# Optimization experiments

Hardware: AMD Instinct MI355X
Metric: run time of the kernel (lower is better)

## Reference

```python
import jax, jax.numpy as jnp
import numpy as np

N, E, B = 4096, 32768, 64
F_IN, E_FEAT, D, D3, G = 128, 64, 64, 64, 10
L = 3           # gc_count
SIG = 0.15      # prior_sig
LAMDA = 0.01    # DiffGroupNorm lambda
EPS = 1e-5      # BatchNorm eps


def setup_inputs() -> dict:
    key = jax.random.key(0)
    ks = jax.random.split(key, 24)
    u = lambda k, shape, s=0.02: jax.random.uniform(k, shape, jnp.float32, -s, s)
    return {
        "x": jax.random.normal(ks[0], (N, F_IN), jnp.float32),
        "edge_attr": jax.random.normal(ks[1], (E, E_FEAT), jnp.float32),
        "pre_W": u(ks[2], (F_IN, D)),
        "pre_b": u(ks[3], (D,)),
        "edge_w1": u(ks[4], (L, E_FEAT, D3), 0.1),
        "edge_b1": u(ks[5], (L, D3), 0.1),
        "edge_w2": u(ks[6], (L, D3, D * D), 0.05),
        "edge_b2": u(ks[7], (L, D * D), 0.05),
        "root_w": u(ks[8], (L, D, D), 0.1),
        "root_b": u(ks[9], (L, D), 0.1),
        "gru_wih": u(ks[10], (L, 3 * D, D), 0.1),
        "gru_whh": u(ks[11], (L, 3 * D, D), 0.1),
        "gru_bih": u(ks[12], (L, 3 * D), 0.1),
        "gru_bhh": u(ks[13], (L, 3 * D), 0.1),
        "gn_lin": u(ks[14], (L, D, G), 0.1),
        "gn_gamma": jnp.ones((L, G * D), jnp.float32),
        "gn_beta": jnp.zeros((L, G * D), jnp.float32),
        "post_W": u(ks[15], (D, D)),
        "post_b": u(ks[16], (D,)),
        "out_W": u(ks[17], (D, 1)),
        "out_b": u(ks[18], (1,)),
        "edge_index": jax.random.randint(ks[19], (2, E), 0, N),
        "batch": jnp.sort(jax.random.randint(ks[20], (N,), 0, B)),
    }


def _kld_det(W, b):
    # BayesLinear forward with sample=False: closed-form prior term
    logc = jnp.log(SIG * jnp.sqrt(2.0 * np.pi))
    return (0.5 * (W / SIG) ** 2 + logc).sum() + (0.5 * (b / SIG) ** 2 + logc).sum()


def _seg_mean(v, idx, num):
    s = jax.ops.segment_sum(v, idx, num_segments=num)
    c = jax.ops.segment_sum(jnp.ones((v.shape[0],), v.dtype), idx, num_segments=num)
    return s / jnp.clip(c, 1.0)[:, None]


def _gru_cell(m, h, wih, whh, bih, bhh):
    # torch GRU gate order: r, z, n
    gi = m @ wih.T + bih          # [N, 3D]
    gh = h @ whh.T + bhh
    i_r, i_z, i_n = jnp.split(gi, 3, axis=-1)
    h_r, h_z, h_n = jnp.split(gh, 3, axis=-1)
    r = jax.nn.sigmoid(i_r + h_r)
    z = jax.nn.sigmoid(i_z + h_z)
    n = jnp.tanh(i_n + r * h_n)
    return (1.0 - z) * n + z * h


def _diff_group_norm(m, lin, gamma, beta):
    # PyG DiffGroupNorm: x + lamda * sum_g s[:,g] * BN(s*x)
    s = jax.nn.softmax(m @ lin, axis=-1)           # [N, G]
    t = (s[:, :, None] * m[:, None, :]).reshape(m.shape[0], G * D)  # [N, G*D]
    mu = t.mean(axis=0)
    var = t.var(axis=0)                            # biased, as BatchNorm1d training
    tn = (t - mu) / jnp.sqrt(var + EPS) * gamma + beta
    return m + LAMDA * tn.reshape(m.shape[0], G, D).sum(axis=1)


def reference(x, edge_attr, pre_W, pre_b, edge_w1, edge_b1, edge_w2, edge_b2,
              root_w, root_b, gru_wih, gru_whh, gru_bih, gru_bhh,
              gn_lin, gn_gamma, gn_beta, post_W, post_b, out_W, out_b,
              edge_index, batch):
    src, dst = edge_index[0], edge_index[1]

    # pre FC (BayesLinear, sample=False) + relu
    out = jax.nn.relu(x @ pre_W + pre_b)
    tkl = _kld_det(pre_W, pre_b)
    prev = out
    h = out                                         # GRU hidden state

    for i in range(L):
        # edge-conditioned weights: MLP(edge_attr) -> [E, D, D]
        We = (jax.nn.relu(edge_attr @ edge_w1[i] + edge_b1[i]) @ edge_w2[i]
              + edge_b2[i]).reshape(E, D, D)
        msg = jnp.einsum('ef,efo->eo', out[src], We)        # gather + per-edge matmul
        agg = _seg_mean(msg, dst, N)                        # scatter-mean
        m = agg + out @ root_w[i] + root_b[i]               # NNConv root weight + bias
        m = _diff_group_norm(m, gn_lin[i], gn_gamma[i], gn_beta[i])
        m = jax.nn.relu(m)
        h = _gru_cell(m, h, gru_wih[i], gru_whh[i], gru_bih[i], gru_bhh[i])
        out = h + prev                                      # residual
        prev = out

    # early global_mean_pool over graphs
    pooled = _seg_mean(out, batch, B)                       # [B, D]
    p = jax.nn.relu(pooled @ post_W + post_b)
    tkl = tkl + _kld_det(post_W, post_b)
    y = p @ out_W + out_b                                   # [B, 1]
    tkl = tkl + _kld_det(out_W, out_b)
    return y.reshape(-1), tkl
```

## Files before the change

### kernel.cpp

```cpp
#include <hip/hip_runtime.h>
#include <math.h>

#define Nn 4096
#define Ee 32768
#define Bb 64
#define FINc 128
#define Dd 64
#define SIGf 0.15f
#define LAMf 0.01f
#define EPSf 1e-5f

typedef __attribute__((ext_vector_type(8))) short bf16x8;
typedef __attribute__((ext_vector_type(4))) float f32x4;

__device__ inline short f2bf(float f) {
  union { float f; unsigned u; } v; v.f = f;
  unsigned r = v.u + 0x7fffu + ((v.u >> 16) & 1u);
  return (short)(r >> 16);
}
__device__ inline float bf2f(unsigned short s) {
  union { unsigned u; float f; } v; v.u = ((unsigned)s) << 16; return v.f;
}
__device__ inline bf16x8 pack8v(f32x4 a, f32x4 b) {
  bf16x8 r;
  r[0]=f2bf(a.x); r[1]=f2bf(a.y); r[2]=f2bf(a.z); r[3]=f2bf(a.w);
  r[4]=f2bf(b.x); r[5]=f2bf(b.y); r[6]=f2bf(b.z); r[7]=f2bf(b.w);
  return r;
}
__device__ inline float sigm(float x) { return 1.f / (1.f + expf(-x)); }

__global__ void k_tkl(const float* __restrict__ preW, const float* __restrict__ preb,
                      const float* __restrict__ postW, const float* __restrict__ postb,
                      const float* __restrict__ outW, const float* __restrict__ outb,
                      float* __restrict__ y) {
  int tid = threadIdx.x;
  const float logc = logf(SIGf * sqrtf(6.28318530717958647692f));
  const float c2 = 0.5f / (SIGf * SIGf);
  float acc = 0.f;
  for (int i = tid; i < FINc*Dd; i += 256) { float w = preW[i];  acc += c2*w*w + logc; }
  for (int i = tid; i < Dd; i += 256)      { float w = preb[i];  acc += c2*w*w + logc; }
  for (int i = tid; i < Dd*Dd; i += 256)   { float w = postW[i]; acc += c2*w*w + logc; }
  for (int i = tid; i < Dd; i += 256)      { float w = postb[i]; acc += c2*w*w + logc; }
  for (int i = tid; i < Dd; i += 256)      { float w = outW[i];  acc += c2*w*w + logc; }
  if (tid == 0)                            { float w = outb[0];  acc += c2*w*w + logc; }
  __shared__ float red[256];
  red[tid] = acc; __syncthreads();
  for (int s = 128; s > 0; s >>= 1) { if (tid < s) red[tid] += red[tid+s]; __syncthreads(); }
  if (tid == 0) y[Bb] = red[0];
}

__global__ void k_count(const int* __restrict__ dst, float* __restrict__ cnt) {
  int e = blockIdx.x * 256 + threadIdx.x;
  if (e < Ee) atomicAdd(&cnt[dst[e]], 1.0f);
}

__global__ void k_prep(const float* __restrict__ w1, const float* __restrict__ w2,
                       const float* __restrict__ b2, const float* __restrict__ rootw,
                       const float* __restrict__ gwih, const float* __restrict__ gwhh,
                       const float* __restrict__ preW,
                       short* __restrict__ w1T, short* __restrict__ b2T,
                       short* __restrict__ w2T, short* __restrict__ rootwT,
                       short* __restrict__ gwihB, short* __restrict__ gwhhB,
                       short* __restrict__ preWT) {
  int idx = blockIdx.x * 256 + threadIdx.x;
  if (idx < 3*64*64*64) {
    int f = idx & 63, o = (idx >> 6) & 63, h = (idx >> 12) & 63, l = idx >> 18;
    w2T[idx] = f2bf(w2[(((l*64 + h)*64 + f) << 6) + o]);
  }
  if (idx < 3*64*64) {
    int f = idx & 63, h = (idx >> 6) & 63, l = idx >> 12;
    w1T[idx] = f2bf(w1[l*4096 + f*64 + h]);
    b2T[idx] = f2bf(b2[l*4096 + f*64 + h]);
    rootwT[idx] = f2bf(rootw[l*4096 + f*64 + h]);
  }
  if (idx < 3*192*64) {
    gwihB[idx] = f2bf(gwih[idx]);
    gwhhB[idx] = f2bf(gwhh[idx]);
  }
  if (idx < 64*128) {
    int k = idx & 127, d = idx >> 7;
    preWT[idx] = f2bf(preW[k*64 + d]);
  }
}

__global__ __launch_bounds__(256) void k_pre(const float* __restrict__ x,
                                             const short* __restrict__ preWT,
                                             const float* __restrict__ preb,
                                             float* __restrict__ out, float* __restrict__ h) {
  const int tid = threadIdx.x, lane = tid & 63, wave = tid >> 6;
  const int m15 = lane & 15, kq = lane >> 4;
  const int nb = blockIdx.x * 16;
  const f32x4 zero4 = {0.f,0.f,0.f,0.f};
  const int d = wave*16 + m15;
  bf16x8 bfr[4];
  #pragma unroll
  for (int c = 0; c < 4; ++c)
    bfr[c] = *(const bf16x8*)(preWT + d*128 + c*32 + kq*8);
  const float* xp = x + (size_t)(nb + m15)*128 + kq*8;
  f32x4 p = zero4;
  #pragma unroll
  for (int c = 0; c < 4; ++c) {
    bf16x8 a = pack8v(*(const f32x4*)(xp + c*32), *(const f32x4*)(xp + c*32 + 4));
    p = __builtin_amdgcn_mfma_f32_16x16x32_bf16(a, bfr[c], p, 0, 0, 0);
  }
  float bv = preb[d];
  #pragma unroll
  for (int r = 0; r < 4; ++r) {
    int node = nb + kq*4 + r;
    float v = fmaxf(p[r] + bv, 0.f);
    out[node*64 + d] = v;
    h[node*64 + d] = v;
  }
}

__global__ __launch_bounds__(512) void k_msg(
    const float* __restrict__ out, const float* __restrict__ edge_attr,
    const short* __restrict__ w1T, const float* __restrict__ b1,
    const short* __restrict__ w2T, const short* __restrict__ b2T,
    const int* __restrict__ src, const int* __restrict__ dst,
    float* __restrict__ agg) {
  __shared__ short hidT[64*520];
  __shared__ __align__(16) short wstage[8192];
  __shared__ int srcv[512];
  __shared__ int dstv[512];

  const int tid  = threadIdx.x;
  const int lane = tid & 63;
  const int w    = tid >> 6;
  const int m15  = lane & 15;
  const int kq   = lane >> 4;
  const int ebi  = blockIdx.x & 63;
  const int os   = blockIdx.x >> 6;
  const int ebase = ebi * 512;
  const int we   = w*64;

  srcv[tid] = src[ebase + tid];
  dstv[tid] = dst[ebase + tid];
  __syncthreads();

  const f32x4 zero4 = {0.f, 0.f, 0.f, 0.f};

  const short* pg0 = w2T + (size_t)w*4096 + os*1024;
  f32x4 s0 = *(const f32x4*)(pg0 + lane*16);
  f32x4 s1 = *(const f32x4*)(pg0 + lane*16 + 8);
  const int wb0 = (lane*32) ^ ((((lane*32) >> 7) & 7) << 4);
  const int wb1 = (lane*32 + 16) ^ ((((lane*32) >> 7) & 7) << 4);

  bf16x8 sfrag[4][2];
  #pragma unroll
  for (int t = 0; t < 4; ++t) {
    int node = srcv[we + t*16 + m15];
    const float* sp = out + node*64 + kq*8;
    #pragma unroll
    for (int ks = 0; ks < 2; ++ks)
      sfrag[t][ks] = pack8v(*(const f32x4*)(sp + ks*32), *(const f32x4*)(sp + ks*32 + 4));
  }

  {
    bf16x8 ea[4][2];
    #pragma unroll
    for (int t = 0; t < 4; ++t) {
      const float* ep = edge_attr + (size_t)(ebase + we + t*16 + m15)*64 + kq*8;
      ea[t][0] = pack8v(*(const f32x4*)(ep),      *(const f32x4*)(ep + 4));
      ea[t][1] = pack8v(*(const f32x4*)(ep + 32), *(const f32x4*)(ep + 36));
    }
    #pragma unroll
    for (int hg = 0; hg < 4; ++hg) {
      const short* wp = w1T + (hg*16 + m15)*64 + kq*8;
      bf16x8 bw0 = *(const bf16x8*)(wp);
      bf16x8 bw1 = *(const bf16x8*)(wp + 32);
      float b1v = b1[hg*16 + m15];
      #pragma unroll
      for (int t = 0; t < 4; ++t) {
        f32x4 p = __builtin_amdgcn_mfma_f32_16x16x32_bf16(ea[t][0], bw0, zero4, 0, 0, 0);
        p = __builtin_amdgcn_mfma_f32_16x16x32_bf16(ea[t][1], bw1, p, 0, 0, 0);
        #pragma unroll
        for (int r = 0; r < 4; ++r)
          hidT[(hg*16 + m15)*520 + we + t*16 + kq*4 + r] = f2bf(fmaxf(p[r] + b1v, 0.f));
      }
    }
  }

  f32x4 acc[4] = {zero4, zero4, zero4, zero4};
  const int ro0 = (m15*128 + kq*16) ^ ((m15 & 7) << 4);
  const int ro1 = (m15*128 + 64 + kq*16) ^ ((m15 & 7) << 4);

  for (int c = 0; c < 8; ++c) {
    __syncthreads();
    {
      char* wd = (char*)wstage + w*2048;
      *(f32x4*)(wd + wb0) = s0;
      *(f32x4*)(wd + wb1) = s1;
    }
    __syncthreads();
    if (c < 7) {
      const short* pg = w2T + (size_t)((c + 1)*8 + w)*4096 + os*1024;
      s0 = *(const f32x4*)(pg + lane*16);
      s1 = *(const f32x4*)(pg + lane*16 + 8);
    }
    #pragma unroll 2
    for (int j = 0; j < 8; ++j) {
      const char* wbp = (const char*)wstage + j*2048;
      bf16x8 W0 = *(const bf16x8*)(wbp + ro0);
      bf16x8 W1 = *(const bf16x8*)(wbp + ro1);
      const unsigned short* hrow =
          (const unsigned short*)hidT + (c*8 + j)*520 + we + kq*4;
      #pragma unroll
      for (int t = 0; t < 4; ++t) {
        f32x4 p = __builtin_amdgcn_mfma_f32_16x16x32_bf16(sfrag[t][0], W0, zero4, 0, 0, 0);
        p = __builtin_amdgcn_mfma_f32_16x16x32_bf16(sfrag[t][1], W1, p, 0, 0, 0);
        ushort4 hu = *(const ushort4*)(hrow + t*16);
        acc[t].x += bf2f(hu.x) * p.x;
        acc[t].y += bf2f(hu.y) * p.y;
        acc[t].z += bf2f(hu.z) * p.z;
        acc[t].w += bf2f(hu.w) * p.w;
      }
    }
  }

  {
    const short* Bp = b2T + (os*16 + m15)*64 + kq*8;
    bf16x8 W0 = *(const bf16x8*)(Bp);
    bf16x8 W1 = *(const bf16x8*)(Bp + 32);
    #pragma unroll
    for (int t = 0; t < 4; ++t) {
      f32x4 p = __builtin_amdgcn_mfma_f32_16x16x32_bf16(sfrag[t][0], W0, zero4, 0, 0, 0);
      p = __builtin_amdgcn_mfma_f32_16x16x32_bf16(sfrag[t][1], W1, p, 0, 0, 0);
      acc[t] += p;
    }
  }

  #pragma unroll
  for (int t = 0; t < 4; ++t) {
    #pragma unroll
    for (int r = 0; r < 4; ++r) {
      int e = we + t*16 + kq*4 + r;
      atomicAdd(&agg[((size_t)os*Nn + dstv[e])*16 + m15], acc[t][r]);
    }
  }
}

__global__ __launch_bounds__(256) void k_m_fused(
    const float* __restrict__ agg, const float* __restrict__ cnt,
    const float* __restrict__ out, const short* __restrict__ rootwT,
    const float* __restrict__ rootb, const float* __restrict__ gnlin,
    float* __restrict__ m, float* __restrict__ sbuf, float* __restrict__ stats) {
  __shared__ float msh[16*65];
  __shared__ float lgsh[16*12];
  __shared__ float ssh[16*16];
  const int tid = threadIdx.x, lane = tid & 63, wave = tid >> 6;
  const int m15 = lane & 15, kq = lane >> 4;
  const int nb = blockIdx.x * 16;
  const f32x4 zero4 = {0.f,0.f,0.f,0.f};
  const int d = wave*16 + m15;

  bf16x8 b0 = *(const bf16x8*)(rootwT + d*64 + kq*8);
  bf16x8 b1 = *(const bf16x8*)(rootwT + d*64 + 32 + kq*8);
  float rbv = rootb[d];
  {
    const float* sp = out + (size_t)(nb + m15)*64 + kq*8;
    bf16x8 a0 = pack8v(*(const f32x4*)(sp),      *(const f32x4*)(sp + 4));
    bf16x8 a1 = pack8v(*(const f32x4*)(sp + 32), *(const f32x4*)(sp + 36));
    f32x4 p = __builtin_amdgcn_mfma_f32_16x16x32_bf16(a0, b0, zero4, 0, 0, 0);
    p = __builtin_amdgcn_mfma_f32_16x16x32_bf16(a1, b1, p, 0, 0, 0);
    #pragma unroll
    for (int r = 0; r < 4; ++r) {
      int ln = kq*4 + r;
      int node = nb + ln;
      float av = agg[((size_t)wave*Nn + node)*16 + m15];
      float mv = av / fmaxf(cnt[node], 1.f) + rbv + p[r];
      m[node*64 + d] = mv;
      msh[ln*65 + d] = mv;
    }
  }
  __syncthreads();

  {
    int n = tid >> 4, g = tid & 15;
    if (g < 10) {
      float lg = 0.f;
      #pragma unroll 8
      for (int k = 0; k < 64; ++k) lg += msh[n*65 + k] * gnlin[k*10 + g];
      lgsh[n*12 + g] = lg;
    }
  }
  __syncthreads();
  {
    int n = tid >> 4, g = tid & 15;
    if (g < 10) {
      float mx = -1e30f;
      #pragma unroll
      for (int gg = 0; gg < 10; ++gg) mx = fmaxf(mx, lgsh[n*12 + gg]);
      float sum = 0.f;
      #pragma unroll
      for (int gg = 0; gg < 10; ++gg) sum += expf(lgsh[n*12 + gg] - mx);
      float sv = expf(lgsh[n*12 + g] - mx) / sum;
      sbuf[(nb + n)*16 + g] = sv;
      ssh[n*16 + g] = sv;
    }
  }
  __syncthreads();
  for (int c = tid; c < 640; c += 256) {
    int g = c >> 6, dd = c & 63;
    float a1 = 0.f, a2 = 0.f;
    #pragma unroll
    for (int n = 0; n < 16; ++n) {
      float t = ssh[n*16 + g] * msh[n*65 + dd];
      a1 += t; a2 += t*t;
    }
    atomicAdd(&stats[c], a1);
    atomicAdd(&stats[640 + c], a2);
  }
}

__global__ __launch_bounds__(256) void k_gru(
    const float* __restrict__ m, const float* __restrict__ sbuf,
    const float* __restrict__ stats, const float* __restrict__ gamma,
    const float* __restrict__ beta, const short* __restrict__ gwihB,
    const short* __restrict__ gwhhB, const float* __restrict__ bih,
    const float* __restrict__ bhh, float* __restrict__ h,
    float* __restrict__ out,
    const int* __restrict__ batch, float* __restrict__ pooled,
    float* __restrict__ pcnt, int doPool) {
  __shared__ __align__(16) float mrsh[16*68];
  __shared__ float igsh[640];
  __shared__ float Bsh[64];
  __shared__ float ssh[256];
  const int tid = threadIdx.x, lane = tid & 63, wave = tid >> 6;
  const int m15 = lane & 15, kq = lane >> 4;
  const int nb = blockIdx.x * 16;
  const f32x4 zero4 = {0.f,0.f,0.f,0.f};
  const float invN = 1.f / (float)Nn;

  if (tid < 64) {
    float bacc = 0.f;
    #pragma unroll
    for (int g = 0; g < 10; ++g) {
      int c = g*64 + tid;
      float mu = stats[c] * invN;
      float var = stats[640 + c] * invN - mu*mu;
      float ig = (1.0f / sqrtf(var + EPSf)) * gamma[c];
      igsh[c] = ig;
      bacc += beta[c] - mu * ig;
    }
    Bsh[tid] = bacc;
  }
  ssh[tid] = sbuf[nb*16 + tid];
  __syncthreads();

  for (int idx = tid; idx < 1024; idx += 256) {
    int n = idx >> 6, dd = idx & 63;
    float mv = m[(nb + n)*64 + dd];
    float SA = 0.f;
    #pragma unroll
    for (int g = 0; g < 10; ++g) SA += ssh[n*16 + g] * igsh[g*64 + dd];
    mrsh[n*68 + dd] = fmaxf(mv * (1.f + LAMf*SA) + LAMf*Bsh[dd], 0.f);
  }
  __syncthreads();

  bf16x8 mrf[2], hf[2];
  {
    const float* mp = mrsh + m15*68 + kq*8;
    const float* hp = h + (size_t)(nb + m15)*64 + kq*8;
    #pragma unroll
    for (int ks = 0; ks < 2; ++ks) {
      mrf[ks] = pack8v(*(const f32x4*)(mp + ks*32), *(const f32x4*)(mp + ks*32 + 4));
      hf[ks]  = pack8v(*(const f32x4*)(hp + ks*32), *(const f32x4*)(hp + ks*32 + 4));
    }
  }
  const int d = wave*16 + m15;
  f32x4 gi[3], gh[3];
  #pragma unroll
  for (int p = 0; p < 3; ++p) {
    int j = p*64 + d;
    bf16x8 bi0 = *(const bf16x8*)(gwihB + j*64 + kq*8);
    bf16x8 bi1 = *(const bf16x8*)(gwihB + j*64 + 32 + kq*8);
    bf16x8 bh0 = *(const bf16x8*)(gwhhB + j*64 + kq*8);
    bf16x8 bh1 = *(const bf16x8*)(gwhhB + j*64 + 32 + kq*8);
    f32x4 a = __builtin_amdgcn_mfma_f32_16x16x32_bf16(mrf[0], bi0, zero4, 0, 0, 0);
    gi[p] = __builtin_amdgcn_mfma_f32_16x16x32_bf16(mrf[1], bi1, a, 0, 0, 0);
    f32x4 b = __builtin_amdgcn_mfma_f32_16x16x32_bf16(hf[0], bh0, zero4, 0, 0, 0);
    gh[p] = __builtin_amdgcn_mfma_f32_16x16x32_bf16(hf[1], bh1, b, 0, 0, 0);
  }
  float bir = bih[d],      bhr = bhh[d];
  float biz = bih[64 + d], bhz = bhh[64 + d];
  float bin = bih[128 + d], bhn = bhh[128 + d];
  __syncthreads();
  #pragma unroll
  for (int r = 0; r < 4; ++r) {
    int node = nb + kq*4 + r;
    float rr = sigm(gi[0][r] + bir + gh[0][r] + bhr);
    float z  = sigm(gi[1][r] + biz + gh[1][r] + bhz);
    float nn = tanhf(gi[2][r] + bin + rr * (gh[2][r] + bhn));
    float hv = h[node*64 + d];
    float hn = (1.f - z) * nn + z * hv;
    h[node*64 + d] = hn;
    float ov = hn + out[node*64 + d];
    out[node*64 + d] = ov;
    if (doPool) {
      int b = batch[node];
      atomicAdd(&pooled[b*64 + d], ov);
      if (d == 0) atomicAdd(&pcnt[b], 1.f);
    }
  }
}

__global__ void k_final(const float* __restrict__ pooled, const float* __restrict__ pcnt,
                        const float* __restrict__ postW, const float* __restrict__ postb,
                        const float* __restrict__ outW, const float* __restrict__ outb,
                        float* __restrict__ y) {
  int b = blockIdx.x, d = threadIdx.x;
  __shared__ float pl[64];
  float c = fmaxf(pcnt[b], 1.f);
  pl[d] = pooled[b*64 + d] / c;
  __syncthreads();
  float acc = postb[d];
  #pragma unroll 8
  for (int k = 0; k < 64; ++k) acc += pl[k] * postW[k*64 + d];
  acc = fmaxf(acc, 0.f);
  float v = acc * outW[d];
  #pragma unroll
  for (int off = 32; off > 0; off >>= 1) v += __shfl_down(v, off, 64);
  if (d == 0) y[b] = v + outb[0];
}

extern "C" void kernel_launch(void* const* d_in, const int* in_sizes, int n_in,
                              void* d_out, int out_size, void* d_ws, size_t ws_size,
                              hipStream_t stream) {
  (void)in_sizes; (void)n_in; (void)out_size; (void)ws_size;
  const float* x        = (const float*)d_in[0];
  const float* edge_attr= (const float*)d_in[1];
  const float* preW     = (const float*)d_in[2];
  const float* preb     = (const float*)d_in[3];
  const float* ew1      = (const float*)d_in[4];
  const float* eb1      = (const float*)d_in[5];
  const float* ew2      = (const float*)d_in[6];
  const float* eb2      = (const float*)d_in[7];
  const float* rootw    = (const float*)d_in[8];
  const float* rootb    = (const float*)d_in[9];
  const float* gwih     = (const float*)d_in[10];
  const float* gwhh     = (const float*)d_in[11];
  const float* gbih     = (const float*)d_in[12];
  const float* gbhh     = (const float*)d_in[13];
  const float* gnlin    = (const float*)d_in[14];
  const float* gngamma  = (const float*)d_in[15];
  const float* gnbeta   = (const float*)d_in[16];
  const float* postW    = (const float*)d_in[17];
  const float* postb    = (const float*)d_in[18];
  const float* outW     = (const float*)d_in[19];
  const float* outb     = (const float*)d_in[20];
  const int*   eidx     = (const int*)d_in[21];
  const int*   batch    = (const int*)d_in[22];
  const int* src = eidx;
  const int* dst = eidx + Ee;
  float* y = (float*)d_out;

  float* ws     = (float*)d_ws;
  float* out    = ws;
  float* hbuf   = out    + Nn*64;
  float* mbuf   = hbuf   + Nn*64;
  float* sbuf   = mbuf   + Nn*64;
  float* agg    = sbuf   + Nn*16;
  float* stats  = agg    + Nn*64;
  float* cnt    = stats  + 2048;
  float* pooled = cnt    + Nn;
  float* pcnt   = pooled + Nn;
  float* bfbase = pcnt   + 64;
  short* w1T    = (short*)bfbase;
  short* b2T    = w1T    + 3*4096;
  short* w2T    = b2T    + 3*4096;
  short* rootwT = w2T    + 3*262144;
  short* gwihB  = rootwT + 3*4096;
  short* gwhhB  = gwihB  + 3*12288;
  short* preWT  = gwhhB  + 3*12288;

  hipMemsetAsync(cnt, 0, (Nn + Nn + 64)*sizeof(float), stream);

  k_prep<<<3072, 256, 0, stream>>>(ew1, ew2, eb2, rootw, gwih, gwhh, preW,
                                   w1T, b2T, w2T, rootwT, gwihB, gwhhB, preWT);
  k_tkl<<<1, 256, 0, stream>>>(preW, preb, postW, postb, outW, outb, y);
  k_count<<<Ee/256, 256, 0, stream>>>(dst, cnt);
  k_pre<<<Nn/16, 256, 0, stream>>>(x, preWT, preb, out, hbuf);

  for (int i = 0; i < 3; ++i) {
    hipMemsetAsync(agg, 0, (Nn*64 + 2048)*sizeof(float), stream);
    k_msg<<<(Ee/512)*4, 512, 0, stream>>>(out, edge_attr,
                                     w1T + i*4096, eb1 + i*64,
                                     w2T + i*262144, b2T + i*4096,
                                     src, dst, agg);
    k_m_fused<<<Nn/16, 256, 0, stream>>>(agg, cnt, out, rootwT + i*4096,
                                         rootb + i*64, gnlin + i*640, mbuf, sbuf, stats);
    k_gru<<<Nn/16, 256, 0, stream>>>(mbuf, sbuf, stats, gngamma + i*640, gnbeta + i*640,
                                     gwihB + i*12288, gwhhB + i*12288,
                                     gbih + i*192, gbhh + i*192, hbuf, out,
                                     batch, pooled, pcnt, (i == 2) ? 1 : 0);
  }

  k_final<<<Bb, 64, 0, stream>>>(pooled, pcnt, postW, postb, outW, outb, y);
}
```

Baseline: 324.5 us.

## Merge prep kernels, shrink message blocks, and drop per-layer memsets

```diff
diff --git a/kernel.cpp b/kernel.cpp
--- a/kernel.cpp
+++ b/kernel.cpp
@@ -29,57 +29,68 @@
 }
 __device__ inline float sigm(float x) { return 1.f / (1.f + expf(-x)); }
 
-__global__ void k_tkl(const float* __restrict__ preW, const float* __restrict__ preb,
-                      const float* __restrict__ postW, const float* __restrict__ postb,
-                      const float* __restrict__ outW, const float* __restrict__ outb,
-                      float* __restrict__ y) {
-  int tid = threadIdx.x;
-  const float logc = logf(SIGf * sqrtf(6.28318530717958647692f));
-  const float c2 = 0.5f / (SIGf * SIGf);
-  float acc = 0.f;
-  for (int i = tid; i < FINc*Dd; i += 256) { float w = preW[i];  acc += c2*w*w + logc; }
-  for (int i = tid; i < Dd; i += 256)      { float w = preb[i];  acc += c2*w*w + logc; }
-  for (int i = tid; i < Dd*Dd; i += 256)   { float w = postW[i]; acc += c2*w*w + logc; }
-  for (int i = tid; i < Dd; i += 256)      { float w = postb[i]; acc += c2*w*w + logc; }
-  for (int i = tid; i < Dd; i += 256)      { float w = outW[i];  acc += c2*w*w + logc; }
-  if (tid == 0)                            { float w = outb[0];  acc += c2*w*w + logc; }
+__global__ __launch_bounds__(256) void k_prep(
+    const float* __restrict__ w1, const float* __restrict__ w2,
+    const float* __restrict__ b2, const float* __restrict__ rootw,
+    const float* __restrict__ gwih, const float* __restrict__ gwhh,
+    const float* __restrict__ preW, const float* __restrict__ preb,
+    const float* __restrict__ postW, const float* __restrict__ postb,
+    const float* __restrict__ outW, const float* __restrict__ outb,
+    const int* __restrict__ dstIdx,
+    short* __restrict__ w1T, short* __restrict__ b2T,
+    short* __restrict__ w2T, short* __restrict__ rootwT,
+    short* __restrict__ gwihB, short* __restrict__ gwhhB,
+    short* __restrict__ preWT, float* __restrict__ cnt,
+    float* __restrict__ y) {
+  const int tid = threadIdx.x;
+  const int bid = blockIdx.x;
+  __shared__ float tile[64][65];
   __shared__ float red[256];
-  red[tid] = acc; __syncthreads();
-  for (int s = 128; s > 0; s >>= 1) { if (tid < s) red[tid] += red[tid+s]; __syncthreads(); }
-  if (tid == 0) y[Bb] = red[0];
-}
-
-__global__ void k_count(const int* __restrict__ dst, float* __restrict__ cnt) {
-  int e = blockIdx.x * 256 + threadIdx.x;
-  if (e < Ee) atomicAdd(&cnt[dst[e]], 1.0f);
-}
-
-__global__ void k_prep(const float* __restrict__ w1, const float* __restrict__ w2,
-                       const float* __restrict__ b2, const float* __restrict__ rootw,
-                       const float* __restrict__ gwih, const float* __restrict__ gwhh,
-                       const float* __restrict__ preW,
-                       short* __restrict__ w1T, short* __restrict__ b2T,
-                       short* __restrict__ w2T, short* __restrict__ rootwT,
-                       short* __restrict__ gwihB, short* __restrict__ gwhhB,
-                       short* __restrict__ preWT) {
-  int idx = blockIdx.x * 256 + threadIdx.x;
-  if (idx < 3*64*64*64) {
-    int f = idx & 63, o = (idx >> 6) & 63, h = (idx >> 12) & 63, l = idx >> 18;
-    w2T[idx] = f2bf(w2[(((l*64 + h)*64 + f) << 6) + o]);
-  }
-  if (idx < 3*64*64) {
-    int f = idx & 63, h = (idx >> 6) & 63, l = idx >> 12;
-    w1T[idx] = f2bf(w1[l*4096 + f*64 + h]);
-    b2T[idx] = f2bf(b2[l*4096 + f*64 + h]);
-    rootwT[idx] = f2bf(rootw[l*4096 + f*64 + h]);
-  }
-  if (idx < 3*192*64) {
-    gwihB[idx] = f2bf(gwih[idx]);
-    gwhhB[idx] = f2bf(gwhh[idx]);
-  }
-  if (idx < 64*128) {
-    int k = idx & 127, d = idx >> 7;
-    preWT[idx] = f2bf(preW[k*64 + d]);
+
+  if (bid < 192) {
+    const float* srcp = w2 + (size_t)bid*4096;
+    #pragma unroll
+    for (int r = 0; r < 16; ++r) {
+      int i2 = r*256 + tid;
+      tile[i2 >> 6][i2 & 63] = srcp[i2];
+    }
+    __syncthreads();
+    short* dstp = w2T + (size_t)bid*4096;
+    #pragma unroll
+    for (int r = 0; r < 16; ++r) {
+      int i2 = r*256 + tid;
+      dstp[i2] = f2bf(tile[i2 & 63][i2 >> 6]);
+    }
+  } else if (bid < 336) {
+    int idx = (bid - 192)*256 + tid;
+    if (idx < 3*64*64) {
+      int f = idx & 63, h = (idx >> 6) & 63, l = idx >> 12;
+      w1T[idx] = f2bf(w1[l*4096 + f*64 + h]);
+      b2T[idx] = f2bf(b2[l*4096 + f*64 + h]);
+      rootwT[idx] = f2bf(rootw[l*4096 + f*64 + h]);
+    }
+    if (idx < 3*192*64) {
+      gwihB[idx] = f2bf(gwih[idx]);
+      gwhhB[idx] = f2bf(gwhh[idx]);
+    }
+    if (idx < 64*128) {
+      int k = idx & 127, d = idx >> 7;
+      preWT[idx] = f2bf(preW[k*64 + d]);
+    }
+    if (idx < Ee) atomicAdd(&cnt[dstIdx[idx]], 1.0f);
+  } else {
+    const float logc = logf(SIGf * sqrtf(6.28318530717958647692f));
+    const float c2 = 0.5f / (SIGf * SIGf);
+    float acc = 0.f;
+    for (int i = tid; i < FINc*Dd; i += 256) { float w = preW[i];  acc += c2*w*w + logc; }
+    for (int i = tid; i < Dd; i += 256)      { float w = preb[i];  acc += c2*w*w + logc; }
+    for (int i = tid; i < Dd*Dd; i += 256)   { float w = postW[i]; acc += c2*w*w + logc; }
+    for (int i = tid; i < Dd; i += 256)      { float w = postb[i]; acc += c2*w*w + logc; }
+    for (int i = tid; i < Dd; i += 256)      { float w = outW[i];  acc += c2*w*w + logc; }
+    if (tid == 0)                            { float w = outb[0];  acc += c2*w*w + logc; }
+    red[tid] = acc; __syncthreads();
+    for (int s = 128; s > 0; s >>= 1) { if (tid < s) red[tid] += red[tid+s]; __syncthreads(); }
+    if (tid == 0) y[Bb] = red[0];
   }
 }
 
@@ -113,36 +124,44 @@
   }
 }
 
-__global__ __launch_bounds__(512) void k_msg(
+__global__ __launch_bounds__(128) void k_msg(
     const float* __restrict__ out, const float* __restrict__ edge_attr,
     const short* __restrict__ w1T, const float* __restrict__ b1,
     const short* __restrict__ w2T, const short* __restrict__ b2T,
     const int* __restrict__ src, const int* __restrict__ dst,
-    float* __restrict__ agg) {
-  __shared__ short hidT[64*520];
+    float* __restrict__ agg, float* __restrict__ stats) {
+  __shared__ short hidT[64*136];
   __shared__ __align__(16) short wstage[8192];
-  __shared__ int srcv[512];
-  __shared__ int dstv[512];
+  __shared__ int srcv[128];
+  __shared__ int dstv[128];
 
   const int tid  = threadIdx.x;
   const int lane = tid & 63;
   const int w    = tid >> 6;
   const int m15  = lane & 15;
   const int kq   = lane >> 4;
-  const int ebi  = blockIdx.x & 63;
-  const int os   = blockIdx.x >> 6;
-  const int ebase = ebi * 512;
+  const int ebi  = blockIdx.x & 255;
+  const int os   = blockIdx.x >> 8;
+  const int ebase = ebi * 128;
   const int we   = w*64;
 
   srcv[tid] = src[ebase + tid];
   dstv[tid] = dst[ebase + tid];
+  if (blockIdx.x == 0) {
+    for (int i = tid; i < 1280; i += 128) stats[i] = 0.f;
+  }
   __syncthreads();
 
   const f32x4 zero4 = {0.f, 0.f, 0.f, 0.f};
 
-  const short* pg0 = w2T + (size_t)w*4096 + os*1024;
-  f32x4 s0 = *(const f32x4*)(pg0 + lane*16);
-  f32x4 s1 = *(const f32x4*)(pg0 + lane*16 + 8);
+  f32x4 s0, s1, s2, s3, s4, s5, s6, s7;
+  {
+    const short* pg = w2T + (size_t)(w*4)*4096 + os*1024 + lane*16;
+    s0 = *(const f32x4*)(pg);          s1 = *(const f32x4*)(pg + 8);
+    s2 = *(const f32x4*)(pg + 4096);   s3 = *(const f32x4*)(pg + 4104);
+    s4 = *(const f32x4*)(pg + 8192);   s5 = *(const f32x4*)(pg + 8200);
+    s6 = *(const f32x4*)(pg + 12288);  s7 = *(const f32x4*)(pg + 12296);
+  }
   const int wb0 = (lane*32) ^ ((((lane*32) >> 7) & 7) << 4);
   const int wb1 = (lane*32 + 16) ^ ((((lane*32) >> 7) & 7) << 4);
 
@@ -174,9 +193,12 @@
       for (int t = 0; t < 4; ++t) {
         f32x4 p = __builtin_amdgcn_mfma_f32_16x16x32_bf16(ea[t][0], bw0, zero4, 0, 0, 0);
         p = __builtin_amdgcn_mfma_f32_16x16x32_bf16(ea[t][1], bw1, p, 0, 0, 0);
-        #pragma unroll
-        for (int r = 0; r < 4; ++r)
-          hidT[(hg*16 + m15)*520 + we + t*16 + kq*4 + r] = f2bf(fmaxf(p[r] + b1v, 0.f));
+        ushort4 hp4;
+        hp4.x = (unsigned short)f2bf(fmaxf(p.x + b1v, 0.f));
+        hp4.y = (unsigned short)f2bf(fmaxf(p.y + b1v, 0.f));
+        hp4.z = (unsigned short)f2bf(fmaxf(p.z + b1v, 0.f));
+        hp4.w = (unsigned short)f2bf(fmaxf(p.w + b1v, 0.f));
+        *(ushort4*)(hidT + (hg*16 + m15)*136 + we + t*16 + kq*4) = hp4;
       }
     }
   }
@@ -188,15 +210,19 @@
   for (int c = 0; c < 8; ++c) {
     __syncthreads();
     {
-      char* wd = (char*)wstage + w*2048;
-      *(f32x4*)(wd + wb0) = s0;
-      *(f32x4*)(wd + wb1) = s1;
+      char* wd = (char*)wstage + (w*4)*2048;
+      *(f32x4*)(wd + wb0) = s0;          *(f32x4*)(wd + wb1) = s1;
+      *(f32x4*)(wd + 2048 + wb0) = s2;   *(f32x4*)(wd + 2048 + wb1) = s3;
+      *(f32x4*)(wd + 4096 + wb0) = s4;   *(f32x4*)(wd + 4096 + wb1) = s5;
+      *(f32x4*)(wd + 6144 + wb0) = s6;   *(f32x4*)(wd + 6144 + wb1) = s7;
     }
     __syncthreads();
     if (c < 7) {
-      const short* pg = w2T + (size_t)((c + 1)*8 + w)*4096 + os*1024;
-      s0 = *(const f32x4*)(pg + lane*16);
-      s1 = *(const f32x4*)(pg + lane*16 + 8);
+      const short* pg = w2T + (size_t)((c + 1)*8 + w*4)*4096 + os*1024 + lane*16;
+      s0 = *(const f32x4*)(pg);          s1 = *(const f32x4*)(pg + 8);
+      s2 = *(const f32x4*)(pg + 4096);   s3 = *(const f32x4*)(pg + 4104);
+      s4 = *(const f32x4*)(pg + 8192);   s5 = *(const f32x4*)(pg + 8200);
+      s6 = *(const f32x4*)(pg + 12288);  s7 = *(const f32x4*)(pg + 12296);
     }
     #pragma unroll 2
     for (int j = 0; j < 8; ++j) {
@@ -204,7 +230,7 @@
       bf16x8 W0 = *(const bf16x8*)(wbp + ro0);
       bf16x8 W1 = *(const bf16x8*)(wbp + ro1);
       const unsigned short* hrow =
-          (const unsigned short*)hidT + (c*8 + j)*520 + we + kq*4;
+          (const unsigned short*)hidT + (c*8 + j)*136 + we + kq*4;
       #pragma unroll
       for (int t = 0; t < 4; ++t) {
         f32x4 p = __builtin_amdgcn_mfma_f32_16x16x32_bf16(sfrag[t][0], W0, zero4, 0, 0, 0);
@@ -241,7 +267,7 @@
 }
 
 __global__ __launch_bounds__(256) void k_m_fused(
-    const float* __restrict__ agg, const float* __restrict__ cnt,
+    float* __restrict__ agg, const float* __restrict__ cnt,
     const float* __restrict__ out, const short* __restrict__ rootwT,
     const float* __restrict__ rootb, const float* __restrict__ gnlin,
     float* __restrict__ m, float* __restrict__ sbuf, float* __restrict__ stats) {
@@ -267,7 +293,9 @@
     for (int r = 0; r < 4; ++r) {
       int ln = kq*4 + r;
       int node = nb + ln;
-      float av = agg[((size_t)wave*Nn + node)*16 + m15];
+      size_t ai = ((size_t)wave*Nn + node)*16 + m15;
+      float av = agg[ai];
+      agg[ai] = 0.f;
       float mv = av / fmaxf(cnt[node], 1.f) + rbv + p[r];
       m[node*64 + d] = mv;
       msh[ln*65 + d] = mv;
@@ -474,20 +502,19 @@
   short* gwhhB  = gwihB  + 3*12288;
   short* preWT  = gwhhB  + 3*12288;
 
-  hipMemsetAsync(cnt, 0, (Nn + Nn + 64)*sizeof(float), stream);
-
-  k_prep<<<3072, 256, 0, stream>>>(ew1, ew2, eb2, rootw, gwih, gwhh, preW,
-                                   w1T, b2T, w2T, rootwT, gwihB, gwhhB, preWT);
-  k_tkl<<<1, 256, 0, stream>>>(preW, preb, postW, postb, outW, outb, y);
-  k_count<<<Ee/256, 256, 0, stream>>>(dst, cnt);
+  hipMemsetAsync(agg, 0, (Nn*64 + 2048 + Nn + Nn + 64)*sizeof(float), stream);
+
+  k_prep<<<337, 256, 0, stream>>>(ew1, ew2, eb2, rootw, gwih, gwhh, preW, preb,
+                                  postW, postb, outW, outb, dst,
+                                  w1T, b2T, w2T, rootwT, gwihB, gwhhB, preWT,
+                                  cnt, y);
   k_pre<<<Nn/16, 256, 0, stream>>>(x, preWT, preb, out, hbuf);
 
   for (int i = 0; i < 3; ++i) {
-    hipMemsetAsync(agg, 0, (Nn*64 + 2048)*sizeof(float), stream);
-    k_msg<<<(Ee/512)*4, 512, 0, stream>>>(out, edge_attr,
+    k_msg<<<(Ee/128)*4, 128, 0, stream>>>(out, edge_attr,
                                      w1T + i*4096, eb1 + i*64,
                                      w2T + i*262144, b2T + i*4096,
-                                     src, dst, agg);
+                                     src, dst, agg, stats);
     k_m_fused<<<Nn/16, 256, 0, stream>>>(agg, cnt, out, rootwT + i*4096,
                                          rootb + i*64, gnlin + i*640, mbuf, sbuf, stats);
     k_gru<<<Nn/16, 256, 0, stream>>>(mbuf, sbuf, stats, gngamma + i*640, gnbeta + i*640,
```

New measurement: 309.0 us (median of 2 runs). 4.8% less time.
